# Kernel optimization log

Hardware: AMD Instinct MI355X
Metric: run time of the kernel (lower is better)

The kernel has to match this reference:

```python
import jax, jax.numpy as jnp
import numpy as np


def mesa_head(xh, yh, qh, lam):
    # xh = per-head 'inputs' (v_proj output), yh = 'targets' (k_proj output),
    # qh = queries; all [T, d]. lam is this head's scalar lambda.
    T, d = xh.shape
    init_inv = jnp.eye(d, dtype=xh.dtype) * lam

    def step(inv, tok):
        x_t, q_t = tok
        Hx = inv @ x_t                      # [d]   (cur_inverse @ x)
        xH = x_t @ inv                      # [d]   (x^T @ cur_inverse)
        denom = 1.0 + x_t @ Hx              # scalar: forward=1 + x^T H x
        new_inv = inv - jnp.outer(Hx, xH) / denom   # Sherman-Morrison rank-1 update
        return new_inv, new_inv @ q_t       # pred_t = S_t @ q_t

    _, preds = jax.lax.scan(step, init_inv, (xh, qh))  # preds: [T, d]

    # scaled_dot_product_attention(preds, xh, yh) with masked=True,
    # use_softmax=False, normalization=False: tril-masked linear attention.
    logits = preds @ xh.T                               # [T, T]
    mask = jnp.tril(jnp.ones((T, T), dtype=bool))
    logits = jnp.where(mask, logits, jnp.zeros((), dtype=logits.dtype))
    return logits @ yh                                  # [T, d]


def reference(x, Wq, Wk, Wv, Wo, lambdas):
    B, T, E = x.shape
    H = lambdas.shape[0]
    d = Wq.shape[1] // H
    q = (x @ Wq).reshape(B, T, H, d)   # query_heads
    k = (x @ Wk).reshape(B, T, H, d)   # target_heads
    v = (x @ Wv).reshape(B, T, H, d)   # input_heads
    # Original call: mesa(input_heads, target_heads, query_heads, lambdas, norm)
    over_batch = jax.vmap(mesa_head, in_axes=(0, 0, 0, None))
    over_heads = jax.vmap(over_batch, in_axes=(2, 2, 2, 0), out_axes=-1)
    mesa_out = over_heads(v, k, q, lambdas)             # [B, T, d, H]
    # Faithful to original: reshape combines (d, H) in that order before o_proj.
    out = mesa_out.reshape(B, T, H * d) @ Wo            # [B, T, E]
    return out


def setup_inputs() -> dict:
    key = jax.random.key(0)
    ks = jax.random.split(key, 6)
    B, T, E, H, d = 2, 1024, 512, 8, 64
    s_in = 1.0 / np.sqrt(E).astype(np.float32)
    s_out = 1.0 / np.sqrt(H * d).astype(np.float32)
    return {
        "x": jax.random.normal(ks[0], (B, T, E), dtype=jnp.float32),
        "Wq": jax.random.normal(ks[1], (E, H * d), dtype=jnp.float32) * s_in,
        "Wk": jax.random.normal(ks[2], (E, H * d), dtype=jnp.float32) * s_in,
        "Wv": jax.random.normal(ks[3], (E, H * d), dtype=jnp.float32) * s_in,
        "Wo": jax.random.normal(ks[4], (H * d, E), dtype=jnp.float32) * s_out,
        "lambdas": jnp.ones((H,), dtype=jnp.float32),
    }
```

## Files before the change

### kernel.cpp

```cpp
#include <hip/hip_runtime.h>

#define T_SEQ 1024
#define DH 64
#define NH 8
#define NB 2
#define EMB 512
#define CS 32
#define NCH 32
#define ACH 16
#define NCHAIN 16

typedef __attribute__((ext_vector_type(8))) short bf16x8;
typedef __attribute__((ext_vector_type(4))) float f32x4;

__device__ __forceinline__ int swz4(int r, int c4) {
    return r * 16 + ((c4 ^ (r >> 2)) & 15);
}

__device__ __forceinline__ void fma4(float4& o, float s, const float4& b) {
    o.x += s * b.x; o.y += s * b.y; o.z += s * b.z; o.w += s * b.w;
}

__device__ __forceinline__ ushort f2bf(float f) {
    unsigned u = __float_as_uint(f);
    return (ushort)((u + 0x7FFFu + ((u >> 16) & 1u)) >> 16);
}
__device__ __forceinline__ float bf2f(ushort h) {
    return __uint_as_float(((unsigned)h) << 16);
}
__device__ __forceinline__ void split2(float f, ushort& hi, ushort& lo) {
    hi = f2bf(f);
    lo = f2bf(f - bf2f(hi));
}

__global__ __launch_bounds__(256) void cvt_split(
    const float4* __restrict__ in, ushort4* __restrict__ hi,
    ushort4* __restrict__ lo) {
    int id = blockIdx.x * 256 + threadIdx.x;
    float4 xv = in[id];
    ushort4 h, l;
    split2(xv.x, h.x, l.x);
    split2(xv.y, h.y, l.y);
    split2(xv.z, h.z, l.z);
    split2(xv.w, h.w, l.w);
    hi[id] = h;
    lo[id] = l;
}

__global__ __launch_bounds__(256) void cvt_wt(
    const float* __restrict__ W0, const float* __restrict__ W1,
    const float* __restrict__ W2, ushort* __restrict__ dhi,
    ushort* __restrict__ dlo, int remap) {
    int zz = blockIdx.z;
    const float* W = (zz == 0) ? W0 : (zz == 1) ? W1 : W2;
    ushort* hi = dhi + (size_t)zz * 262144;
    ushort* lo = dlo + (size_t)zz * 262144;
    int kk0 = blockIdx.x * 64, n0 = blockIdx.y * 64;
    __shared__ float T[64][65];
    int t = threadIdx.x;
#pragma unroll
    for (int i = 0; i < 4; ++i) {
        int rl = i * 16 + (t >> 4);
        int rs = remap ? (rl * 8 + (kk0 >> 6)) : (kk0 + rl);
        float4 vv = *(const float4*)&W[(size_t)rs * 512 + n0 + (t & 15) * 4];
        T[rl][(t & 15) * 4 + 0] = vv.x;
        T[rl][(t & 15) * 4 + 1] = vv.y;
        T[rl][(t & 15) * 4 + 2] = vv.z;
        T[rl][(t & 15) * 4 + 3] = vv.w;
    }
    __syncthreads();
    int nl = t >> 2, kl = (t & 3) * 16;
#pragma unroll
    for (int j4 = 0; j4 < 4; ++j4) {
        ushort4 h4, l4;
        split2(T[kl + j4 * 4 + 0][nl], h4.x, l4.x);
        split2(T[kl + j4 * 4 + 1][nl], h4.y, l4.y);
        split2(T[kl + j4 * 4 + 2][nl], h4.z, l4.z);
        split2(T[kl + j4 * 4 + 3][nl], h4.w, l4.w);
        size_t dst = (size_t)(n0 + nl) * 512 + kk0 + kl + j4 * 4;
        *(ushort4*)&hi[dst] = h4;
        *(ushort4*)&lo[dst] = l4;
    }
}

__global__ __launch_bounds__(256) void cvt_ao(
    const float4* __restrict__ ao, ushort4* __restrict__ hi,
    ushort4* __restrict__ lo) {
    int id = blockIdx.x * 256 + threadIdx.x;
    int chain = id >> 14;
    int tt = (id >> 4) & 1023;
    int d4 = id & 15;
    float4 xv = ao[id];
    int m = ((chain >> 3) << 10) + tt;
    int dst = m * 128 + ((chain & 7) << 4) + d4;
    ushort4 h, l;
    split2(xv.x, h.x, l.x);
    split2(xv.y, h.y, l.y);
    split2(xv.z, h.z, l.z);
    split2(xv.w, h.w, l.w);
    hi[dst] = h;
    lo[dst] = l;
}

template <int MODE>
__global__ __launch_bounds__(256) void mfma_gemm(
    const ushort* __restrict__ Ahi, const ushort* __restrict__ Alo,
    const ushort* __restrict__ Bth, const ushort* __restrict__ Btl,
    float* __restrict__ o0, float* __restrict__ o1, float* __restrict__ o2) {
    int bm = blockIdx.x, bn = blockIdx.y, zz = blockIdx.z;
    const ushort* Bh = Bth + (size_t)zz * 262144;
    const ushort* Bl = Btl + (size_t)zz * 262144;
    float* out = (MODE == 0) ? ((zz == 0) ? o0 : (zz == 1) ? o1 : o2) : o0;

    __shared__ ushort Ash[128 * 40];
    __shared__ ushort Asl[128 * 40];
    __shared__ ushort Bsh[64 * 40];
    __shared__ ushort Bsl[64 * 40];

    int tid = threadIdx.x;
    int lane = tid & 63, wid = tid >> 6;
    int wm = wid >> 1, wn = wid & 1;
    int fr = lane & 15, fk = (lane >> 4) * 8;
    int sr = tid >> 2, sc = (tid & 3) * 8;

    f32x4 zero = {0.f, 0.f, 0.f, 0.f};
    f32x4 acc[4][2];
#pragma unroll
    for (int f = 0; f < 4; ++f)
#pragma unroll
        for (int g = 0; g < 2; ++g) acc[f][g] = zero;

    const ushort* gAh = Ahi + (size_t)(bm * 128 + sr) * 512 + sc;
    const ushort* gAl = Alo + (size_t)(bm * 128 + sr) * 512 + sc;
    const ushort* gBh = Bh + (size_t)(bn * 64 + sr) * 512 + sc;
    const ushort* gBl = Bl + (size_t)(bn * 64 + sr) * 512 + sc;

    for (int k0 = 0; k0 < 512; k0 += 32) {
        uint4 a0 = *(const uint4*)(gAh + k0);
        uint4 a1 = *(const uint4*)(gAh + 64 * 512 + k0);
        uint4 a2 = *(const uint4*)(gAl + k0);
        uint4 a3 = *(const uint4*)(gAl + 64 * 512 + k0);
        uint4 b0 = *(const uint4*)(gBh + k0);
        uint4 b1 = *(const uint4*)(gBl + k0);
        __syncthreads();
        *(uint4*)&Ash[sr * 40 + sc] = a0;
        *(uint4*)&Ash[(sr + 64) * 40 + sc] = a1;
        *(uint4*)&Asl[sr * 40 + sc] = a2;
        *(uint4*)&Asl[(sr + 64) * 40 + sc] = a3;
        *(uint4*)&Bsh[sr * 40 + sc] = b0;
        *(uint4*)&Bsl[sr * 40 + sc] = b1;
        __syncthreads();
        bf16x8 ah[4], al[4], bh[2], blo[2];
#pragma unroll
        for (int f = 0; f < 4; ++f) {
            int r = wm * 64 + f * 16 + fr;
            ah[f] = *(const bf16x8*)&Ash[r * 40 + fk];
            al[f] = *(const bf16x8*)&Asl[r * 40 + fk];
        }
#pragma unroll
        for (int g = 0; g < 2; ++g) {
            int r = wn * 32 + g * 16 + fr;
            bh[g] = *(const bf16x8*)&Bsh[r * 40 + fk];
            blo[g] = *(const bf16x8*)&Bsl[r * 40 + fk];
        }
#pragma unroll
        for (int f = 0; f < 4; ++f)
#pragma unroll
            for (int g = 0; g < 2; ++g) {
                acc[f][g] = __builtin_amdgcn_mfma_f32_16x16x32_bf16(
                    ah[f], bh[g], acc[f][g], 0, 0, 0);
                acc[f][g] = __builtin_amdgcn_mfma_f32_16x16x32_bf16(
                    ah[f], blo[g], acc[f][g], 0, 0, 0);
                acc[f][g] = __builtin_amdgcn_mfma_f32_16x16x32_bf16(
                    al[f], bh[g], acc[f][g], 0, 0, 0);
            }
    }

    int rbase = (lane >> 4) * 4;
#pragma unroll
    for (int f = 0; f < 4; ++f)
#pragma unroll
        for (int g = 0; g < 2; ++g)
#pragma unroll
            for (int j = 0; j < 4; ++j) {
                int m = bm * 128 + wm * 64 + f * 16 + rbase + j;
                int n = bn * 64 + wn * 32 + g * 16 + (lane & 15);
                float val = acc[f][g][j];
                if (MODE == 0) {
                    int b = m >> 10, tt = m & 1023;
                    int h = n >> 6, d = n & 63;
                    out[(((size_t)(b * 8 + h) * 1024 + tt) << 6) + d] = val;
                } else {
                    out[(size_t)m * 512 + n] = val;
                }
            }
}

__global__ __launch_bounds__(256) void gram_kernel(
    const float* __restrict__ v, float* __restrict__ g) {
    int chain = blockIdx.x, chunk = blockIdx.y;
    const float* X = v + ((size_t)chain * T_SEQ + chunk * CS) * DH;
    __shared__ float Xs[CS * 64];
    int tid = threadIdx.x;
#pragma unroll
    for (int i = 0; i < (CS * 16) / 256; ++i)
        ((float4*)Xs)[i * 256 + tid] = ((const float4*)X)[i * 256 + tid];
    __syncthreads();

    int tx = tid & 15, ty = tid >> 4;
    float acc[4][4];
#pragma unroll
    for (int i = 0; i < 4; ++i)
#pragma unroll
        for (int j = 0; j < 4; ++j) acc[i][j] = 0.f;

#pragma unroll 4
    for (int t = 0; t < CS; ++t) {
        float a_[4], b_[4];
#pragma unroll
        for (int i = 0; i < 4; ++i) a_[i] = Xs[t * 64 + ty * 4 + i];
#pragma unroll
        for (int j = 0; j < 4; ++j) b_[j] = Xs[t * 64 + tx * 4 + j];
#pragma unroll
        for (int i = 0; i < 4; ++i)
#pragma unroll
            for (int j = 0; j < 4; ++j) acc[i][j] += a_[i] * b_[j];
    }

    float* gp = g + ((size_t)chain * NCH + chunk) * 4096;
#pragma unroll
    for (int i = 0; i < 4; ++i)
        *(float4*)(gp + (ty * 4 + i) * 64 + tx * 4) =
            make_float4(acc[i][0], acc[i][1], acc[i][2], acc[i][3]);
}

__global__ __launch_bounds__(256) void prefix_kernel(float* __restrict__ g) {
    int gid = blockIdx.x * 256 + threadIdx.x;
    int chain = gid >> 12, elem = gid & 4095;
    float* p = g + (size_t)chain * NCH * 4096 + elem;
    float run = 0.f;
#pragma unroll
    for (int c = 0; c < NCH; ++c) {
        float val = p[(size_t)c * 4096];
        p[(size_t)c * 4096] = run;
        run += val;
    }
}

__global__ __launch_bounds__(256) void invscan(
    const float* __restrict__ g, const float* __restrict__ v,
    const float* __restrict__ q, const float* __restrict__ lambdas,
    float* __restrict__ preds) {
    int blk = blockIdx.x;
    int chain = blk >> 5, chunk = blk & 31;
    int tid = threadIdx.x;
    int row = tid >> 2;
    int ch = tid & 3;
    int wav = tid >> 6;
    float lam = lambdas[chain & (NH - 1)];

    __shared__ float pbuf[2][64];
    __shared__ float Xs[CS * 64];
    __shared__ float Qs[CS * 64];
    __shared__ float hxs[2][64];
    __shared__ float red1[2][4], red2[2][4];

    float m[16];
    {
        const float4* gp = (const float4*)(g + (size_t)blk * 4096);
#pragma unroll
        for (int i = 0; i < 4; ++i) {
            float4 t4 = gp[row * 16 + ch * 4 + i];
            m[i * 4 + 0] = t4.x; m[i * 4 + 1] = t4.y;
            m[i * 4 + 2] = t4.z; m[i * 4 + 3] = t4.w;
        }
    }
#pragma unroll
    for (int i = 0; i < 16; ++i)
        if (ch * 16 + i == row) m[i] += lam;

    const float4* vb = (const float4*)(v + ((size_t)chain * T_SEQ + chunk * CS) * DH);
    const float4* qb = (const float4*)(q + ((size_t)chain * T_SEQ + chunk * CS) * DH);
    ((float4*)Xs)[tid] = vb[tid];
    ((float4*)Xs)[256 + tid] = vb[256 + tid];
    ((float4*)Qs)[tid] = qb[tid];
    ((float4*)Qs)[256 + tid] = qb[256 + tid];

    if (row == 0) {
#pragma unroll
        for (int i = 0; i < 16; ++i) pbuf[0][ch * 16 + i] = m[i];
    }
    __syncthreads();

    for (int p = 0; p < 64; ++p) {
        const float* pb = pbuf[p & 1];
        float pr[16];
#pragma unroll
        for (int i = 0; i < 4; ++i) {
            float4 t4 = ((const float4*)pb)[ch * 4 + i];
            pr[i * 4 + 0] = t4.x; pr[i * 4 + 1] = t4.y;
            pr[i * 4 + 2] = t4.z; pr[i * 4 + 3] = t4.w;
        }
        float diag = pb[p];
        float gcv = pb[row];
        float ipiv = 1.f / diag;
        if (row == p) {
#pragma unroll
            for (int i = 0; i < 16; ++i)
                m[i] = (ch * 16 + i == p) ? -ipiv : pr[i] * ipiv;
        } else {
            float beta = gcv * ipiv;
#pragma unroll
            for (int i = 0; i < 16; ++i)
                m[i] = (ch * 16 + i == p) ? beta : m[i] - beta * pr[i];
        }
        if (p < 63 && row == p + 1) {
#pragma unroll
            for (int i = 0; i < 16; ++i) pbuf[(p + 1) & 1][ch * 16 + i] = m[i];
        }
        __syncthreads();
    }

    float* pbo = preds + ((size_t)chain * T_SEQ + chunk * CS) * DH;
    for (int t = 0; t < CS; ++t) {
        int par = t & 1;
        float hx = 0.f, hq = 0.f;
#pragma unroll
        for (int i = 0; i < 4; ++i) {
            float4 x4 = ((const float4*)(Xs + t * 64))[ch * 4 + i];
            float4 q4 = ((const float4*)(Qs + t * 64))[ch * 4 + i];
            hx += m[i * 4 + 0] * x4.x + m[i * 4 + 1] * x4.y +
                  m[i * 4 + 2] * x4.z + m[i * 4 + 3] * x4.w;
            hq += m[i * 4 + 0] * q4.x + m[i * 4 + 1] * q4.y +
                  m[i * 4 + 2] * q4.z + m[i * 4 + 3] * q4.w;
        }
        hx += __shfl_xor(hx, 1); hx += __shfl_xor(hx, 2);
        hq += __shfl_xor(hq, 1); hq += __shfl_xor(hq, 2);
        float Hx = -hx, Hq = -hq;

        float xr = Xs[t * 64 + row];
        float qr = Qs[t * 64 + row];
        float s1 = xr * Hx, s2 = qr * Hx;
#pragma unroll
        for (int off = 32; off; off >>= 1) {
            s1 += __shfl_xor(s1, off);
            s2 += __shfl_xor(s2, off);
        }
        if ((tid & 63) == 0) { red1[par][wav] = s1; red2[par][wav] = s2; }
        if (ch == 0) hxs[par][row] = Hx;
        __syncthreads();
        float p1 = 0.25f * (red1[par][0] + red1[par][1] + red1[par][2] + red1[par][3]);
        float p2 = 0.25f * (red2[par][0] + red2[par][1] + red2[par][2] + red2[par][3]);
        float idn = 1.f / (1.f + p1);
        if (ch == 0) pbo[(size_t)t * DH + row] = Hq - Hx * (p2 * idn);

        float coef = Hx * idn;
#pragma unroll
        for (int i = 0; i < 4; ++i) {
            float4 h4 = ((const float4*)hxs[par])[ch * 4 + i];
            m[i * 4 + 0] += coef * h4.x; m[i * 4 + 1] += coef * h4.y;
            m[i * 4 + 2] += coef * h4.z; m[i * 4 + 3] += coef * h4.w;
        }
    }
}

__global__ __launch_bounds__(256) void kv_gram(
    const float* __restrict__ V, const float* __restrict__ Kv,
    float* __restrict__ D) {
    int chain = blockIdx.x, ck = blockIdx.y;
    __shared__ float Vs[64 * 64];
    __shared__ float Ks2[64 * 64];
    int tid = threadIdx.x;
    const float4* Vb = (const float4*)(V + ((size_t)chain * T_SEQ + ck * 64) * DH);
    const float4* Kb = (const float4*)(Kv + ((size_t)chain * T_SEQ + ck * 64) * DH);
#pragma unroll
    for (int i = 0; i < 4; ++i) {
        ((float4*)Vs)[i * 256 + tid] = Vb[i * 256 + tid];
        ((float4*)Ks2)[i * 256 + tid] = Kb[i * 256 + tid];
    }
    __syncthreads();

    int tx = tid & 15, ty = tid >> 4;
    float acc[4][4];
#pragma unroll
    for (int i = 0; i < 4; ++i)
#pragma unroll
        for (int j = 0; j < 4; ++j) acc[i][j] = 0.f;

#pragma unroll 4
    for (int t = 0; t < 64; ++t) {
        float a_[4], b_[4];
#pragma unroll
        for (int i = 0; i < 4; ++i) a_[i] = Vs[t * 64 + ty * 4 + i];
#pragma unroll
        for (int j = 0; j < 4; ++j) b_[j] = Ks2[t * 64 + tx * 4 + j];
#pragma unroll
        for (int i = 0; i < 4; ++i)
#pragma unroll
            for (int j = 0; j < 4; ++j) acc[i][j] += a_[i] * b_[j];
    }

    float* dp = D + ((size_t)chain * ACH + ck) * 4096;
#pragma unroll
    for (int i = 0; i < 4; ++i)
        *(float4*)(dp + (ty * 4 + i) * 64 + tx * 4) =
            make_float4(acc[i][0], acc[i][1], acc[i][2], acc[i][3]);
}

__global__ __launch_bounds__(256) void kv_prefix(float* __restrict__ d) {
    int gid = blockIdx.x * 256 + threadIdx.x;
    int chain = gid >> 12, elem = gid & 4095;
    float* p = d + (size_t)chain * ACH * 4096 + elem;
    float run = 0.f;
#pragma unroll
    for (int c = 0; c < ACH; ++c) {
        float val = p[(size_t)c * 4096];
        p[(size_t)c * 4096] = run;
        run += val;
    }
}

__global__ __launch_bounds__(256) void attn_chunk(
    const float* __restrict__ P, const float* __restrict__ V,
    const float* __restrict__ Kv, const float* __restrict__ C,
    float* __restrict__ O) {
    int ck = blockIdx.x, bh = blockIdx.y;
    int tid = threadIdx.x, tx = tid & 15, ty = tid >> 4;

    __shared__ float4 Ps[64 * 16];
    __shared__ float4 Bs[64 * 16];
    __shared__ float4 Ks[64 * 16];

    int lr = tid >> 2, lc = tid & 3;
    const float4* Pb = (const float4*)(P + ((size_t)bh * T_SEQ + ck * 64) * DH);
    const float4* Vb = (const float4*)(V + ((size_t)bh * T_SEQ + ck * 64) * DH);
    const float4* Kb = (const float4*)(Kv + ((size_t)bh * T_SEQ + ck * 64) * DH);
    const float4* Cb = (const float4*)(C + ((size_t)bh * ACH + ck) * 4096);
#pragma unroll
    for (int i = 0; i < 4; ++i) {
        Ps[swz4(lr, lc + i * 4)] = Pb[lr * 16 + lc + i * 4];
        Bs[swz4(lr, lc + i * 4)] = Cb[lr * 16 + lc + i * 4];
        Ks[swz4(lr, lc + i * 4)] = Kb[lr * 16 + lc + i * 4];
    }

    float4 o[4];
    o[0] = o[1] = o[2] = o[3] = make_float4(0.f, 0.f, 0.f, 0.f);
    __syncthreads();

    const float* Pf = (const float*)Ps;
#pragma unroll 4
    for (int j = 0; j < 64; ++j) {
        float4 b4 = Bs[swz4(j, tx)];
#pragma unroll
        for (int i = 0; i < 4; ++i) {
            float s = Pf[swz4(ty * 4 + i, j >> 2) * 4 + (j & 3)];
            fma4(o[i], s, b4);
        }
    }
    __syncthreads();

#pragma unroll
    for (int i = 0; i < 4; ++i)
        Bs[swz4(lr, lc + i * 4)] = Vb[lr * 16 + lc + i * 4];
    __syncthreads();

    float4 sa[4][4];
#pragma unroll
    for (int i = 0; i < 4; ++i)
#pragma unroll
        for (int j = 0; j < 4; ++j) sa[i][j] = make_float4(0.f, 0.f, 0.f, 0.f);
#pragma unroll
    for (int d4 = 0; d4 < 16; ++d4) {
        float4 a[4], b[4];
#pragma unroll
        for (int i = 0; i < 4; ++i) a[i] = Ps[swz4(ty * 4 + i, d4)];
#pragma unroll
        for (int j = 0; j < 4; ++j) b[j] = Bs[swz4(tx * 4 + j, d4)];
#pragma unroll
        for (int i = 0; i < 4; ++i)
#pragma unroll
            for (int j = 0; j < 4; ++j) {
                sa[i][j].x += a[i].x * b[j].x;
                sa[i][j].y += a[i].y * b[j].y;
                sa[i][j].z += a[i].z * b[j].z;
                sa[i][j].w += a[i].w * b[j].w;
            }
    }
    __syncthreads();

#pragma unroll
    for (int i = 0; i < 4; ++i) {
        int m = ty * 4 + i;
        float sv[4];
#pragma unroll
        for (int j = 0; j < 4; ++j) {
            float s = sa[i][j].x + sa[i][j].y + sa[i][j].z + sa[i][j].w;
            if ((tx * 4 + j) > m) s = 0.f;
            sv[j] = s;
        }
        Bs[swz4(m, tx)] = make_float4(sv[0], sv[1], sv[2], sv[3]);
    }
    __syncthreads();

    const float* Sf = (const float*)Bs;
#pragma unroll 4
    for (int j = 0; j < 64; ++j) {
        float4 b4 = Ks[swz4(j, tx)];
#pragma unroll
        for (int i = 0; i < 4; ++i) {
            float s = Sf[swz4(ty * 4 + i, j >> 2) * 4 + (j & 3)];
            fma4(o[i], s, b4);
        }
    }

#pragma unroll
    for (int i = 0; i < 4; ++i) {
        float* dst = O + ((size_t)bh * T_SEQ + ck * 64 + ty * 4 + i) * DH + tx * 4;
        *(float4*)dst = o[i];
    }
}

extern "C" void kernel_launch(void* const* d_in, const int* in_sizes, int n_in,
                              void* d_out, int out_size, void* d_ws, size_t ws_size,
                              hipStream_t stream) {
    const float* x = (const float*)d_in[0];
    const float* Wq = (const float*)d_in[1];
    const float* Wk = (const float*)d_in[2];
    const float* Wv = (const float*)d_in[3];
    const float* Wo = (const float*)d_in[4];
    const float* lambdas = (const float*)d_in[5];
    float* out = (float*)d_out;

    float* ws = (float*)d_ws;
    const size_t SZ = (size_t)NB * NH * T_SEQ * DH;
    float* q = ws;
    float* k = ws + SZ;
    float* v = ws + 2 * SZ;
    float* preds = ws + 3 * SZ;
    ushort* x_hi = (ushort*)(ws + 3 * SZ);
    ushort* x_lo = (ushort*)(ws + 3 * SZ + SZ / 2);
    ushort* A2_hi = x_hi;
    ushort* A2_lo = x_lo;
    float* g = ws + 4 * SZ;
    ushort* Wt_hi = (ushort*)(ws + 4 * SZ);
    ushort* Wt_lo = (ushort*)(ws + 4 * SZ + 393216);
    float* dbuf = g;
    float* ao = g + SZ;
    ushort* Wot_hi = (ushort*)(ws + 4 * SZ);
    ushort* Wot_lo = (ushort*)(ws + 4 * SZ + 131072);

    cvt_split<<<dim3(1024), 256, 0, stream>>>(
        (const float4*)x, (ushort4*)x_hi, (ushort4*)x_lo);
    cvt_wt<<<dim3(8, 8, 3), 256, 0, stream>>>(Wq, Wk, Wv, Wt_hi, Wt_lo, 0);
    mfma_gemm<0><<<dim3(16, 8, 3), 256, 0, stream>>>(
        x_hi, x_lo, Wt_hi, Wt_lo, q, k, v);
    gram_kernel<<<dim3(NCHAIN, NCH), 256, 0, stream>>>(v, g);
    prefix_kernel<<<dim3(256), 256, 0, stream>>>(g);
    invscan<<<dim3(NCHAIN * NCH), 256, 0, stream>>>(g, v, q, lambdas, preds);
    kv_gram<<<dim3(NCHAIN, ACH), 256, 0, stream>>>(v, k, dbuf);
    kv_prefix<<<dim3(256), 256, 0, stream>>>(dbuf);
    attn_chunk<<<dim3(ACH, NCHAIN), 256, 0, stream>>>(preds, v, k, dbuf, ao);
    cvt_ao<<<dim3(1024), 256, 0, stream>>>(
        (const float4*)ao, (ushort4*)A2_hi, (ushort4*)A2_lo);
    cvt_wt<<<dim3(8, 8, 1), 256, 0, stream>>>(Wo, Wo, Wo, Wot_hi, Wot_lo, 1);
    mfma_gemm<1><<<dim3(16, 8, 1), 256, 0, stream>>>(
        A2_hi, A2_lo, Wot_hi, Wot_lo, out, out, out);
}
```

Measured before the change: 145.9 us.

## Split invscan chunks into half-chunks to double block count

Each 32-token chunk of the Sherman-Morrison scan is now handled by two blocks of 16 tokens, which doubles the grid from 512 to 1024 blocks and halves the serial per-token loop. The second-half block rebuilds its starting Gram matrix by adding the first half's 16 outer products to the prefix before inverting. Predictions are staged in shared memory and written out with coalesced float4 stores. The cost is that every block still runs the full 64-pivot Gauss-Jordan inversion, so inversion work doubles, and second-half blocks do extra rank-1 accumulation.

```diff
diff --git a/kernel.cpp b/kernel.cpp
--- a/kernel.cpp
+++ b/kernel.cpp
@@ -6,6 +6,7 @@
 #define NB 2
 #define EMB 512
 #define CS 32
+#define SCS 16
 #define NCH 32
 #define ACH 16
 #define NCHAIN 16
@@ -252,7 +253,9 @@
     const float* __restrict__ q, const float* __restrict__ lambdas,
     float* __restrict__ preds) {
     int blk = blockIdx.x;
-    int chain = blk >> 5, chunk = blk & 31;
+    int chain = blk >> 6, sub = blk & 63;
+    int c32 = sub >> 1, half = sub & 1;
+    int t0 = c32 * CS + half * SCS;
     int tid = threadIdx.x;
     int row = tid >> 2;
     int ch = tid & 3;
@@ -260,14 +263,15 @@
     float lam = lambdas[chain & (NH - 1)];
 
     __shared__ float pbuf[2][64];
-    __shared__ float Xs[CS * 64];
-    __shared__ float Qs[CS * 64];
+    __shared__ float Xs[SCS * 64];
+    __shared__ float Qs[SCS * 64];
+    __shared__ float XhPo[SCS * 64];
     __shared__ float hxs[2][64];
     __shared__ float red1[2][4], red2[2][4];
 
     float m[16];
     {
-        const float4* gp = (const float4*)(g + (size_t)blk * 4096);
+        const float4* gp = (const float4*)(g + ((size_t)chain * NCH + c32) * 4096);
 #pragma unroll
         for (int i = 0; i < 4; ++i) {
             float4 t4 = gp[row * 16 + ch * 4 + i];
@@ -279,13 +283,25 @@
     for (int i = 0; i < 16; ++i)
         if (ch * 16 + i == row) m[i] += lam;
 
-    const float4* vb = (const float4*)(v + ((size_t)chain * T_SEQ + chunk * CS) * DH);
-    const float4* qb = (const float4*)(q + ((size_t)chain * T_SEQ + chunk * CS) * DH);
+    const float4* vb = (const float4*)(v + ((size_t)chain * T_SEQ + t0) * DH);
+    const float4* qb = (const float4*)(q + ((size_t)chain * T_SEQ + t0) * DH);
     ((float4*)Xs)[tid] = vb[tid];
-    ((float4*)Xs)[256 + tid] = vb[256 + tid];
     ((float4*)Qs)[tid] = qb[tid];
-    ((float4*)Qs)[256 + tid] = qb[256 + tid];
-
+    if (half) {
+        const float4* hb = (const float4*)(v + ((size_t)chain * T_SEQ + c32 * CS) * DH);
+        ((float4*)XhPo)[tid] = hb[tid];
+    }
+    __syncthreads();
+
+    if (half) {
+#pragma unroll 4
+        for (int t = 0; t < SCS; ++t) {
+            float xr = XhPo[t * 64 + row];
+#pragma unroll
+            for (int i = 0; i < 16; ++i)
+                m[i] += xr * XhPo[t * 64 + ch * 16 + i];
+        }
+    }
     if (row == 0) {
 #pragma unroll
         for (int i = 0; i < 16; ++i) pbuf[0][ch * 16 + i] = m[i];
@@ -321,8 +337,7 @@
         __syncthreads();
     }
 
-    float* pbo = preds + ((size_t)chain * T_SEQ + chunk * CS) * DH;
-    for (int t = 0; t < CS; ++t) {
+    for (int t = 0; t < SCS; ++t) {
         int par = t & 1;
         float hx = 0.f, hq = 0.f;
 #pragma unroll
@@ -352,7 +367,7 @@
         float p1 = 0.25f * (red1[par][0] + red1[par][1] + red1[par][2] + red1[par][3]);
         float p2 = 0.25f * (red2[par][0] + red2[par][1] + red2[par][2] + red2[par][3]);
         float idn = 1.f / (1.f + p1);
-        if (ch == 0) pbo[(size_t)t * DH + row] = Hq - Hx * (p2 * idn);
+        if (ch == 0) XhPo[t * 64 + row] = Hq - Hx * (p2 * idn);
 
         float coef = Hx * idn;
 #pragma unroll
@@ -362,6 +377,10 @@
             m[i * 4 + 2] += coef * h4.z; m[i * 4 + 3] += coef * h4.w;
         }
     }
+    __syncthreads();
+
+    float4* pbo4 = (float4*)(preds + ((size_t)chain * T_SEQ + t0) * DH);
+    pbo4[tid] = ((const float4*)XhPo)[tid];
 }
 
 __global__ __launch_bounds__(256) void kv_gram(
@@ -556,7 +575,7 @@
         x_hi, x_lo, Wt_hi, Wt_lo, q, k, v);
     gram_kernel<<<dim3(NCHAIN, NCH), 256, 0, stream>>>(v, g);
     prefix_kernel<<<dim3(256), 256, 0, stream>>>(g);
-    invscan<<<dim3(NCHAIN * NCH), 256, 0, stream>>>(g, v, q, lambdas, preds);
+    invscan<<<dim3(NCHAIN * NCH * 2), 256, 0, stream>>>(g, v, q, lambdas, preds);
     kv_gram<<<dim3(NCHAIN, ACH), 256, 0, stream>>>(v, k, dbuf);
     kv_prefix<<<dim3(256), 256, 0, stream>>>(dbuf);
     attn_chunk<<<dim3(ACH, NCHAIN), 256, 0, stream>>>(preds, v, k, dbuf, ao);
```

Measured after the change: 155.0 us. 6.2% more time.

## Block invscan into rank-2 steps and merge conversion kernels into fewer launches

Applied to the files above, without the earlier changes.

The Gauss-Jordan inversion in invscan now eliminates two pivots per iteration, and the token scan applies a rank-2 (Woodbury-style) update per token pair. This halves the number of block-wide barriers in both loops. Predictions are staged in shared memory and written out as coalesced float4 stores. The x/weight and ao/Wo conversion kernels are merged into two launches to cut launch overhead. The trade-off is more registers and arithmetic per step, plus possible numerical differences from 2x2 pivoting without row exchange.

```diff
diff --git a/kernel.cpp b/kernel.cpp
--- a/kernel.cpp
+++ b/kernel.cpp
@@ -33,73 +33,112 @@
     lo = f2bf(f - bf2f(hi));
 }
 
-__global__ __launch_bounds__(256) void cvt_split(
-    const float4* __restrict__ in, ushort4* __restrict__ hi,
-    ushort4* __restrict__ lo) {
-    int id = blockIdx.x * 256 + threadIdx.x;
-    float4 xv = in[id];
-    ushort4 h, l;
-    split2(xv.x, h.x, l.x);
-    split2(xv.y, h.y, l.y);
-    split2(xv.z, h.z, l.z);
-    split2(xv.w, h.w, l.w);
-    hi[id] = h;
-    lo[id] = l;
-}
-
-__global__ __launch_bounds__(256) void cvt_wt(
-    const float* __restrict__ W0, const float* __restrict__ W1,
-    const float* __restrict__ W2, ushort* __restrict__ dhi,
-    ushort* __restrict__ dlo, int remap) {
+__global__ __launch_bounds__(256) void prep_qkv(
+    const float* __restrict__ x, const float* __restrict__ W0,
+    const float* __restrict__ W1, const float* __restrict__ W2,
+    ushort* __restrict__ x_hi, ushort* __restrict__ x_lo,
+    ushort* __restrict__ Wt_hi, ushort* __restrict__ Wt_lo) {
     int zz = blockIdx.z;
-    const float* W = (zz == 0) ? W0 : (zz == 1) ? W1 : W2;
-    ushort* hi = dhi + (size_t)zz * 262144;
-    ushort* lo = dlo + (size_t)zz * 262144;
-    int kk0 = blockIdx.x * 64, n0 = blockIdx.y * 64;
+    int t = threadIdx.x;
     __shared__ float T[64][65];
+    if (zz < 3) {
+        const float* W = (zz == 0) ? W0 : (zz == 1) ? W1 : W2;
+        ushort* hi = Wt_hi + (size_t)zz * 262144;
+        ushort* lo = Wt_lo + (size_t)zz * 262144;
+        int kk0 = blockIdx.x * 64, n0 = blockIdx.y * 64;
+#pragma unroll
+        for (int i = 0; i < 4; ++i) {
+            int rl = i * 16 + (t >> 4);
+            float4 vv = *(const float4*)&W[(size_t)(kk0 + rl) * 512 + n0 + (t & 15) * 4];
+            T[rl][(t & 15) * 4 + 0] = vv.x;
+            T[rl][(t & 15) * 4 + 1] = vv.y;
+            T[rl][(t & 15) * 4 + 2] = vv.z;
+            T[rl][(t & 15) * 4 + 3] = vv.w;
+        }
+        __syncthreads();
+        int nl = t >> 2, kl = (t & 3) * 16;
+#pragma unroll
+        for (int j4 = 0; j4 < 4; ++j4) {
+            ushort4 h4, l4;
+            split2(T[kl + j4 * 4 + 0][nl], h4.x, l4.x);
+            split2(T[kl + j4 * 4 + 1][nl], h4.y, l4.y);
+            split2(T[kl + j4 * 4 + 2][nl], h4.z, l4.z);
+            split2(T[kl + j4 * 4 + 3][nl], h4.w, l4.w);
+            size_t dst = (size_t)(n0 + nl) * 512 + kk0 + kl + j4 * 4;
+            *(ushort4*)&hi[dst] = h4;
+            *(ushort4*)&lo[dst] = l4;
+        }
+    } else {
+        int bid = blockIdx.y * 8 + blockIdx.x;
+        const float4* in = (const float4*)x;
+        ushort4* hi = (ushort4*)x_hi;
+        ushort4* lo = (ushort4*)x_lo;
+#pragma unroll
+        for (int i = 0; i < 16; ++i) {
+            int id = (bid * 16 + i) * 256 + t;
+            float4 xv = in[id];
+            ushort4 h, l;
+            split2(xv.x, h.x, l.x);
+            split2(xv.y, h.y, l.y);
+            split2(xv.z, h.z, l.z);
+            split2(xv.w, h.w, l.w);
+            hi[id] = h;
+            lo[id] = l;
+        }
+    }
+}
+
+__global__ __launch_bounds__(256) void prep_out(
+    const float* __restrict__ Wo, const float4* __restrict__ ao,
+    ushort* __restrict__ Wot_hi, ushort* __restrict__ Wot_lo,
+    ushort4* __restrict__ A2_hi, ushort4* __restrict__ A2_lo) {
     int t = threadIdx.x;
-#pragma unroll
-    for (int i = 0; i < 4; ++i) {
-        int rl = i * 16 + (t >> 4);
-        int rs = remap ? (rl * 8 + (kk0 >> 6)) : (kk0 + rl);
-        float4 vv = *(const float4*)&W[(size_t)rs * 512 + n0 + (t & 15) * 4];
-        T[rl][(t & 15) * 4 + 0] = vv.x;
-        T[rl][(t & 15) * 4 + 1] = vv.y;
-        T[rl][(t & 15) * 4 + 2] = vv.z;
-        T[rl][(t & 15) * 4 + 3] = vv.w;
-    }
-    __syncthreads();
-    int nl = t >> 2, kl = (t & 3) * 16;
-#pragma unroll
-    for (int j4 = 0; j4 < 4; ++j4) {
-        ushort4 h4, l4;
-        split2(T[kl + j4 * 4 + 0][nl], h4.x, l4.x);
-        split2(T[kl + j4 * 4 + 1][nl], h4.y, l4.y);
-        split2(T[kl + j4 * 4 + 2][nl], h4.z, l4.z);
-        split2(T[kl + j4 * 4 + 3][nl], h4.w, l4.w);
-        size_t dst = (size_t)(n0 + nl) * 512 + kk0 + kl + j4 * 4;
-        *(ushort4*)&hi[dst] = h4;
-        *(ushort4*)&lo[dst] = l4;
-    }
-}
-
-__global__ __launch_bounds__(256) void cvt_ao(
-    const float4* __restrict__ ao, ushort4* __restrict__ hi,
-    ushort4* __restrict__ lo) {
-    int id = blockIdx.x * 256 + threadIdx.x;
-    int chain = id >> 14;
-    int tt = (id >> 4) & 1023;
-    int d4 = id & 15;
-    float4 xv = ao[id];
-    int m = ((chain >> 3) << 10) + tt;
-    int dst = m * 128 + ((chain & 7) << 4) + d4;
-    ushort4 h, l;
-    split2(xv.x, h.x, l.x);
-    split2(xv.y, h.y, l.y);
-    split2(xv.z, h.z, l.z);
-    split2(xv.w, h.w, l.w);
-    hi[dst] = h;
-    lo[dst] = l;
+    __shared__ float T[64][65];
+    if (blockIdx.z == 0) {
+        int kk0 = blockIdx.x * 64, n0 = blockIdx.y * 64;
+#pragma unroll
+        for (int i = 0; i < 4; ++i) {
+            int rl = i * 16 + (t >> 4);
+            int rs = rl * 8 + (kk0 >> 6);
+            float4 vv = *(const float4*)&Wo[(size_t)rs * 512 + n0 + (t & 15) * 4];
+            T[rl][(t & 15) * 4 + 0] = vv.x;
+            T[rl][(t & 15) * 4 + 1] = vv.y;
+            T[rl][(t & 15) * 4 + 2] = vv.z;
+            T[rl][(t & 15) * 4 + 3] = vv.w;
+        }
+        __syncthreads();
+        int nl = t >> 2, kl = (t & 3) * 16;
+#pragma unroll
+        for (int j4 = 0; j4 < 4; ++j4) {
+            ushort4 h4, l4;
+            split2(T[kl + j4 * 4 + 0][nl], h4.x, l4.x);
+            split2(T[kl + j4 * 4 + 1][nl], h4.y, l4.y);
+            split2(T[kl + j4 * 4 + 2][nl], h4.z, l4.z);
+            split2(T[kl + j4 * 4 + 3][nl], h4.w, l4.w);
+            size_t dst = (size_t)(n0 + nl) * 512 + kk0 + kl + j4 * 4;
+            *(ushort4*)&Wot_hi[dst] = h4;
+            *(ushort4*)&Wot_lo[dst] = l4;
+        }
+    } else {
+        int bid = blockIdx.y * 8 + blockIdx.x;
+#pragma unroll
+        for (int i = 0; i < 16; ++i) {
+            int id = (bid * 16 + i) * 256 + t;
+            int chain = id >> 14;
+            int tt = (id >> 4) & 1023;
+            int d4 = id & 15;
+            float4 xv = ao[id];
+            int mrow = ((chain >> 3) << 10) + tt;
+            int dst = mrow * 128 + ((chain & 7) << 4) + d4;
+            ushort4 h, l;
+            split2(xv.x, h.x, l.x);
+            split2(xv.y, h.y, l.y);
+            split2(xv.z, h.z, l.z);
+            split2(xv.w, h.w, l.w);
+            A2_hi[dst] = h;
+            A2_lo[dst] = l;
+        }
+    }
 }
 
 template <int MODE>
@@ -254,20 +293,19 @@
     int blk = blockIdx.x;
     int chain = blk >> 5, chunk = blk & 31;
     int tid = threadIdx.x;
-    int row = tid >> 2;
-    int ch = tid & 3;
-    int wav = tid >> 6;
+    int row = tid >> 2, ch = tid & 3, wav = tid >> 6;
     float lam = lambdas[chain & (NH - 1)];
 
-    __shared__ float pbuf[2][64];
+    __shared__ float rbuf[2][64];
+    __shared__ float sbuf[2][64];
     __shared__ float Xs[CS * 64];
     __shared__ float Qs[CS * 64];
-    __shared__ float hxs[2][64];
-    __shared__ float red1[2][4], red2[2][4];
+    __shared__ float Po[CS * 64];
+    __shared__ float red[2][6][4];
 
     float m[16];
     {
-        const float4* gp = (const float4*)(g + (size_t)blk * 4096);
+        const float4* gp = (const float4*)(g + ((size_t)chain * NCH + chunk) * 4096);
 #pragma unroll
         for (int i = 0; i < 4; ++i) {
             float4 t4 = gp[row * 16 + ch * 4 + i];
@@ -288,80 +326,137 @@
 
     if (row == 0) {
 #pragma unroll
-        for (int i = 0; i < 16; ++i) pbuf[0][ch * 16 + i] = m[i];
-    }
-    __syncthreads();
-
-    for (int p = 0; p < 64; ++p) {
-        const float* pb = pbuf[p & 1];
-        float pr[16];
-#pragma unroll
-        for (int i = 0; i < 4; ++i) {
-            float4 t4 = ((const float4*)pb)[ch * 4 + i];
-            pr[i * 4 + 0] = t4.x; pr[i * 4 + 1] = t4.y;
-            pr[i * 4 + 2] = t4.z; pr[i * 4 + 3] = t4.w;
-        }
-        float diag = pb[p];
-        float gcv = pb[row];
-        float ipiv = 1.f / diag;
+        for (int i = 0; i < 4; ++i)
+            ((float4*)rbuf[0])[ch * 4 + i] =
+                make_float4(m[i * 4], m[i * 4 + 1], m[i * 4 + 2], m[i * 4 + 3]);
+    }
+    if (row == 1) {
+#pragma unroll
+        for (int i = 0; i < 4; ++i)
+            ((float4*)sbuf[0])[ch * 4 + i] =
+                make_float4(m[i * 4], m[i * 4 + 1], m[i * 4 + 2], m[i * 4 + 3]);
+    }
+    __syncthreads();
+
+#pragma unroll
+    for (int pp = 0; pp < 32; ++pp) {
+        const int p = 2 * pp;
+        const float* rb = rbuf[pp & 1];
+        const float* sb = sbuf[pp & 1];
+        float r_[16], s_[16];
+#pragma unroll
+        for (int i = 0; i < 4; ++i) {
+            float4 t4 = ((const float4*)rb)[ch * 4 + i];
+            r_[i * 4] = t4.x; r_[i * 4 + 1] = t4.y;
+            r_[i * 4 + 2] = t4.z; r_[i * 4 + 3] = t4.w;
+            float4 u4 = ((const float4*)sb)[ch * 4 + i];
+            s_[i * 4] = u4.x; s_[i * 4 + 1] = u4.y;
+            s_[i * 4 + 2] = u4.z; s_[i * 4 + 3] = u4.w;
+        }
+        float rp = rb[p], rp2 = rb[p + 1], sp2 = sb[p + 1];
+        float gr = rb[row], gs = sb[row];
+        float i1 = 1.f / rp;
+        float al = rp2 * i1;
+        float i2 = 1.f / (sp2 - al * rp2);
+        float c0, ca, cb;
         if (row == p) {
-#pragma unroll
-            for (int i = 0; i < 16; ++i)
-                m[i] = (ch * 16 + i == p) ? -ipiv : pr[i] * ipiv;
+            c0 = 0.f; ca = i1 + al * al * i2; cb = -al * i2;
+        } else if (row == p + 1) {
+            c0 = 0.f; ca = -al * i2; cb = i2;
         } else {
-            float beta = gcv * ipiv;
-#pragma unroll
-            for (int i = 0; i < 16; ++i)
-                m[i] = (ch * 16 + i == p) ? beta : m[i] - beta * pr[i];
-        }
-        if (p < 63 && row == p + 1) {
-#pragma unroll
-            for (int i = 0; i < 16; ++i) pbuf[(p + 1) & 1][ch * 16 + i] = m[i];
+            float b2 = (gs - al * gr) * i2;
+            c0 = 1.f; ca = al * b2 - gr * i1; cb = -b2;
+        }
+#pragma unroll
+        for (int i = 0; i < 16; ++i) m[i] = c0 * m[i] + ca * r_[i] + cb * s_[i];
+        if (ch == (p >> 4)) {
+            m[p & 15] = -ca;
+            m[(p & 15) + 1] = -cb;
+        }
+        if (pp < 31) {
+            if (row == p + 2) {
+#pragma unroll
+                for (int i = 0; i < 4; ++i)
+                    ((float4*)rbuf[(pp + 1) & 1])[ch * 4 + i] =
+                        make_float4(m[i * 4], m[i * 4 + 1], m[i * 4 + 2], m[i * 4 + 3]);
+            }
+            if (row == p + 3) {
+#pragma unroll
+                for (int i = 0; i < 4; ++i)
+                    ((float4*)sbuf[(pp + 1) & 1])[ch * 4 + i] =
+                        make_float4(m[i * 4], m[i * 4 + 1], m[i * 4 + 2], m[i * 4 + 3]);
+            }
         }
         __syncthreads();
     }
 
-    float* pbo = preds + ((size_t)chain * T_SEQ + chunk * CS) * DH;
-    for (int t = 0; t < CS; ++t) {
-        int par = t & 1;
-        float hx = 0.f, hq = 0.f;
-#pragma unroll
-        for (int i = 0; i < 4; ++i) {
-            float4 x4 = ((const float4*)(Xs + t * 64))[ch * 4 + i];
-            float4 q4 = ((const float4*)(Qs + t * 64))[ch * 4 + i];
-            hx += m[i * 4 + 0] * x4.x + m[i * 4 + 1] * x4.y +
-                  m[i * 4 + 2] * x4.z + m[i * 4 + 3] * x4.w;
-            hq += m[i * 4 + 0] * q4.x + m[i * 4 + 1] * q4.y +
-                  m[i * 4 + 2] * q4.z + m[i * 4 + 3] * q4.w;
-        }
-        hx += __shfl_xor(hx, 1); hx += __shfl_xor(hx, 2);
-        hq += __shfl_xor(hq, 1); hq += __shfl_xor(hq, 2);
-        float Hx = -hx, Hq = -hq;
-
-        float xr = Xs[t * 64 + row];
-        float qr = Qs[t * 64 + row];
-        float s1 = xr * Hx, s2 = qr * Hx;
+#pragma unroll
+    for (int tp = 0; tp < 16; ++tp) {
+        const int ta = 2 * tp, tb2 = 2 * tp + 1;
+        const int par = tp & 1;
+        float pu = 0.f, pw = 0.f, pza = 0.f, pzb = 0.f;
+#pragma unroll
+        for (int i = 0; i < 4; ++i) {
+            float4 xa = ((const float4*)(Xs + ta * 64))[ch * 4 + i];
+            float4 xb = ((const float4*)(Xs + tb2 * 64))[ch * 4 + i];
+            float4 qa = ((const float4*)(Qs + ta * 64))[ch * 4 + i];
+            float4 q4 = ((const float4*)(Qs + tb2 * 64))[ch * 4 + i];
+            pu += m[i * 4] * xa.x + m[i * 4 + 1] * xa.y + m[i * 4 + 2] * xa.z + m[i * 4 + 3] * xa.w;
+            pw += m[i * 4] * xb.x + m[i * 4 + 1] * xb.y + m[i * 4 + 2] * xb.z + m[i * 4 + 3] * xb.w;
+            pza += m[i * 4] * qa.x + m[i * 4 + 1] * qa.y + m[i * 4 + 2] * qa.z + m[i * 4 + 3] * qa.w;
+            pzb += m[i * 4] * q4.x + m[i * 4 + 1] * q4.y + m[i * 4 + 2] * q4.z + m[i * 4 + 3] * q4.w;
+        }
+        pu += __shfl_xor(pu, 1); pu += __shfl_xor(pu, 2);
+        pw += __shfl_xor(pw, 1); pw += __shfl_xor(pw, 2);
+        pza += __shfl_xor(pza, 1); pza += __shfl_xor(pza, 2);
+        pzb += __shfl_xor(pzb, 1); pzb += __shfl_xor(pzb, 2);
+        float u = -pu, w = -pw, za = -pza, zb = -pzb;
+        if (ch == 0) rbuf[par][row] = u;
+        if (ch == 1) sbuf[par][row] = w;
+        float a_ = Xs[ta * 64 + row], b_ = Xs[tb2 * 64 + row];
+        float qa_ = Qs[ta * 64 + row], qb_ = Qs[tb2 * 64 + row];
+        float d0 = a_ * u, d1 = b_ * u, d2 = b_ * w;
+        float d3 = qa_ * u, d4 = qb_ * u, d5 = qb_ * w;
 #pragma unroll
         for (int off = 32; off; off >>= 1) {
-            s1 += __shfl_xor(s1, off);
-            s2 += __shfl_xor(s2, off);
-        }
-        if ((tid & 63) == 0) { red1[par][wav] = s1; red2[par][wav] = s2; }
-        if (ch == 0) hxs[par][row] = Hx;
+            d0 += __shfl_xor(d0, off); d1 += __shfl_xor(d1, off);
+            d2 += __shfl_xor(d2, off); d3 += __shfl_xor(d3, off);
+            d4 += __shfl_xor(d4, off); d5 += __shfl_xor(d5, off);
+        }
+        if ((tid & 63) == 0) {
+            red[par][0][wav] = d0; red[par][1][wav] = d1; red[par][2][wav] = d2;
+            red[par][3][wav] = d3; red[par][4][wav] = d4; red[par][5][wav] = d5;
+        }
         __syncthreads();
-        float p1 = 0.25f * (red1[par][0] + red1[par][1] + red1[par][2] + red1[par][3]);
-        float p2 = 0.25f * (red2[par][0] + red2[par][1] + red2[par][2] + red2[par][3]);
-        float idn = 1.f / (1.f + p1);
-        if (ch == 0) pbo[(size_t)t * DH + row] = Hq - Hx * (p2 * idn);
-
-        float coef = Hx * idn;
-#pragma unroll
-        for (int i = 0; i < 4; ++i) {
-            float4 h4 = ((const float4*)hxs[par])[ch * 4 + i];
-            m[i * 4 + 0] += coef * h4.x; m[i * 4 + 1] += coef * h4.y;
-            m[i * 4 + 2] += coef * h4.z; m[i * 4 + 3] += coef * h4.w;
-        }
-    }
+        float saa = 0.25f * (red[par][0][0] + red[par][0][1] + red[par][0][2] + red[par][0][3]);
+        float sab = 0.25f * (red[par][1][0] + red[par][1][1] + red[par][1][2] + red[par][1][3]);
+        float sbb = 0.25f * (red[par][2][0] + red[par][2][1] + red[par][2][2] + red[par][2][3]);
+        float c1  = 0.25f * (red[par][3][0] + red[par][3][1] + red[par][3][2] + red[par][3][3]);
+        float c2  = 0.25f * (red[par][4][0] + red[par][4][1] + red[par][4][2] + red[par][4][3]);
+        float c3  = 0.25f * (red[par][5][0] + red[par][5][1] + red[par][5][2] + red[par][5][3]);
+        float k1 = 1.f / (1.f + saa);
+        float al2 = sab * k1;
+        float k2 = 1.f / (1.f + sbb - sab * al2);
+        float vr = w - al2 * u;
+        if (ch == 0) Po[ta * 64 + row] = za - (c1 * k1) * u;
+        if (ch == 1) Po[tb2 * 64 + row] = zb - (c2 * k1) * u - (k2 * (c3 - al2 * c2)) * vr;
+        float cu = k1 * u - al2 * k2 * vr;
+        float cw = k2 * vr;
+#pragma unroll
+        for (int i = 0; i < 4; ++i) {
+            float4 uj = ((const float4*)rbuf[par])[ch * 4 + i];
+            float4 wj = ((const float4*)sbuf[par])[ch * 4 + i];
+            m[i * 4 + 0] += cu * uj.x + cw * wj.x;
+            m[i * 4 + 1] += cu * uj.y + cw * wj.y;
+            m[i * 4 + 2] += cu * uj.z + cw * wj.z;
+            m[i * 4 + 3] += cu * uj.w + cw * wj.w;
+        }
+    }
+    __syncthreads();
+
+    float4* po4 = (float4*)(preds + ((size_t)chain * T_SEQ + chunk * CS) * DH);
+    po4[tid] = ((const float4*)Po)[tid];
+    po4[256 + tid] = ((const float4*)Po)[256 + tid];
 }
 
 __global__ __launch_bounds__(256) void kv_gram(
@@ -549,9 +644,8 @@
     ushort* Wot_hi = (ushort*)(ws + 4 * SZ);
     ushort* Wot_lo = (ushort*)(ws + 4 * SZ + 131072);
 
-    cvt_split<<<dim3(1024), 256, 0, stream>>>(
-        (const float4*)x, (ushort4*)x_hi, (ushort4*)x_lo);
-    cvt_wt<<<dim3(8, 8, 3), 256, 0, stream>>>(Wq, Wk, Wv, Wt_hi, Wt_lo, 0);
+    prep_qkv<<<dim3(8, 8, 4), 256, 0, stream>>>(x, Wq, Wk, Wv,
+                                                x_hi, x_lo, Wt_hi, Wt_lo);
     mfma_gemm<0><<<dim3(16, 8, 3), 256, 0, stream>>>(
         x_hi, x_lo, Wt_hi, Wt_lo, q, k, v);
     gram_kernel<<<dim3(NCHAIN, NCH), 256, 0, stream>>>(v, g);
@@ -560,9 +654,9 @@
     kv_gram<<<dim3(NCHAIN, ACH), 256, 0, stream>>>(v, k, dbuf);
     kv_prefix<<<dim3(256), 256, 0, stream>>>(dbuf);
     attn_chunk<<<dim3(ACH, NCHAIN), 256, 0, stream>>>(preds, v, k, dbuf, ao);
-    cvt_ao<<<dim3(1024), 256, 0, stream>>>(
-        (const float4*)ao, (ushort4*)A2_hi, (ushort4*)A2_lo);
-    cvt_wt<<<dim3(8, 8, 1), 256, 0, stream>>>(Wo, Wo, Wo, Wot_hi, Wot_lo, 1);
+    prep_out<<<dim3(8, 8, 2), 256, 0, stream>>>(Wo, (const float4*)ao,
+                                                Wot_hi, Wot_lo,
+                                                (ushort4*)A2_hi, (ushort4*)A2_lo);
     mfma_gemm<1><<<dim3(16, 8, 1), 256, 0, stream>>>(
         A2_hi, A2_lo, Wot_hi, Wot_lo, out, out, out);
 }
```

Result: faster. 135.2 us (-7.3%).
